# Kernel tuning notes

Hardware: AMD Instinct MI355X
Metric: run time of the kernel (lower is better)

Reference implementation:

```python
import jax, jax.numpy as jnp
import numpy as np

F32 = jnp.float32

def denorm_px(pts, H, W):
    # kornia denormalize_pixel_coordinates: [-1,1] -> pixel
    x = (pts[..., 0] + 1.0) * (W - 1) * 0.5
    y = (pts[..., 1] + 1.0) * (H - 1) * 0.5
    return jnp.stack([x, y], axis=-1)

def norm_px(pts, H, W):
    x = pts[..., 0] * 2.0 / (W - 1) - 1.0
    y = pts[..., 1] * 2.0 / (H - 1) - 1.0
    return jnp.stack([x, y], axis=-1)

def conv2d_same(x, k, mode):
    # depthwise 2d conv, 'same' output, border via jnp.pad mode
    kh, kw = k.shape
    ph, pw = kh // 2, kw // 2
    xp = jnp.pad(x, ((0, 0), (0, 0), (ph, ph), (pw, pw)), mode=mode)
    C = x.shape[1]
    kern = jnp.broadcast_to(k[None, None], (C, 1, kh, kw)).astype(x.dtype)
    return jax.lax.conv_general_dilated(xp, kern, (1, 1), 'VALID',
        dimension_numbers=('NCHW', 'OIHW', 'NCHW'), feature_group_count=C)

def nms2d(x, k=5):
    p = k // 2
    m = jax.lax.reduce_window(x, -jnp.inf, jax.lax.max, (1, 1, k, k), (1, 1, 1, 1),
                              [(0, 0), (0, 0), (p, p), (p, p)])
    return jnp.where(x == m, x, 0.0)

def gaussian_kernel2d(ksize=7, sigma=1.0):
    ax = jnp.arange(ksize, dtype=F32) - (ksize - 1) / 2.0
    g = jnp.exp(-0.5 * (ax / sigma) ** 2)
    g = g / g.sum()
    return jnp.outer(g, g)

def gftt_response(gray):
    # kornia CornerGFTT: normalized sobel grads, blurred structure tensor, min-eig
    sx = jnp.array([[-1, 0, 1], [-2, 0, 2], [-1, 0, 1]], F32) / 8.0
    gx = conv2d_same(gray, sx, 'edge')
    gy = conv2d_same(gray, sx.T, 'edge')
    g = gaussian_kernel2d(7, 1.0)
    dx2 = conv2d_same(gx * gx, g, 'reflect')
    dy2 = conv2d_same(gy * gy, g, 'reflect')
    dxy = conv2d_same(gx * gy, g, 'reflect')
    tr = dx2 + dy2
    disc = jnp.sqrt(jnp.clip((dx2 - dy2) ** 2 + 4.0 * dxy ** 2, 0.0))
    return 0.5 * (tr - disc)

def laplacian5(x):
    k = jnp.ones((5, 5), F32).at[2, 2].set(1.0 - 25.0)
    k = k / jnp.abs(k).sum()  # kornia normalized laplacian kernel
    return conv2d_same(x, k, 'reflect')

def pairwise_project(pts, depths, poses, K):
    # pts [B,N,2] normalized; poses [B,4,4] cam-to-world
    # returns proj [B(dst),B(src),N,2] normalized + vis [B,B,N]
    B, N, _ = pts.shape
    H, W = depths.shape[-2:]
    px = denorm_px(pts, H, W)
    xi = jnp.clip(jnp.round(px[..., 0]), 0, W - 1).astype(jnp.int32)
    yi = jnp.clip(jnp.round(px[..., 1]), 0, H - 1).astype(jnp.int32)
    d = depths[jnp.arange(B)[:, None], 0, yi, xi]  # [B,N]
    Kinv = jnp.linalg.inv(K)
    hom = jnp.concatenate([px, jnp.ones_like(px[..., :1])], axis=-1)
    cam = (hom @ Kinv.T) * d[..., None]  # [B,N,3]
    R, t = poses[:, :3, :3], poses[:, :3, 3]
    world = jnp.einsum('bij,bnj->bni', R, cam) + t[:, None]
    diff = world[None] - t[:, None, None]  # [i,j,n,3]
    cam2 = jnp.einsum('iab,ijna->ijnb', R, diff)  # R_i^T (world - t_i)
    uvw = cam2 @ K.T
    z = uvw[..., 2]
    zs = jnp.where(jnp.abs(z) > 1e-6, z, 1e-6)
    u, v = uvw[..., 0] / zs, uvw[..., 1] / zs
    vis = (z > 0.1) & (u >= 0) & (u <= W - 1) & (v >= 0) & (v <= H - 1)
    return norm_px(jnp.stack([u, v], -1), H, W), vis

def pairwise_cosine_inter(x, y, eps=1e-8):
    xx = jnp.sum(x * x, -1)
    yy = jnp.sum(y * y, -1)
    xy = jnp.einsum('amd,bnd->abmn', x, y)
    den = jnp.sqrt(jnp.clip(xx[:, None, :, None] * yy[None, :, None, :], eps * eps))
    return xy / den

def pairwise_cosine_intra(x, y, eps=1e-8):
    xx = jnp.sum(x * x, -1)
    yy = jnp.sum(y * y, -1)
    xy = jnp.einsum('bmd,bnd->bmn', x, y)
    den = jnp.sqrt(jnp.clip(xx[..., :, None] * yy[..., None, :], eps * eps))
    return xy / den

def distinction_loss(desc):
    return jnp.maximum(pairwise_cosine_intra(desc, desc), 0.0).mean()

def match_loss(desc, points, proj, vis, H, W, radius=1.0):
    B, N, _ = points.shape
    src = denorm_px(jax.lax.stop_gradient(points), H, W)  # [b,m,2]
    dst = denorm_px(jax.lax.stop_gradient(proj), H, W)  # [a,b,n,2]
    x2 = jnp.sum(src * src, -1)  # [b,m]
    y2 = jnp.sum(dst * dst, -1)  # [a,b,n]
    xy = jnp.einsum('bmd,abnd->abmn', src, dst)
    dist = jnp.sqrt(jnp.clip(x2[None, :, :, None] + y2[:, :, None, :] - 2.0 * xy, 0.0))
    valid = vis[:, :, :, None]  # torch: dist[invis rows] = nan -> excluded from both masks
    tri = jnp.triu(jnp.ones((N, N), bool), 1)
    pcos = pairwise_cosine_inter(desc, desc)
    mpos = (dist <= radius) & tri & valid
    mneg = (dist > radius) & tri & valid
    pos_mean = jnp.sum(jnp.where(mpos, pcos, 0.0)) / jnp.maximum(mpos.sum(), 1)
    neg_mean = jnp.sum(jnp.where(mneg, pcos, 0.0)) / jnp.maximum(mneg.sum(), 1)
    return 1.0 - pos_mean + neg_mean

def get_corner_target(imgs, depths, poses, K, num_corners=500, radius=8):
    B, _, H, W = imgs.shape
    gray = 0.299 * imgs[:, 0:1] + 0.587 * imgs[:, 1:2] + 0.114 * imgs[:, 2:3]
    corners = nms2d(gftt_response(gray), 5)
    # MaxPool(8, return_indices) + MaxUnpool(8): keep only per-8x8-block max
    xr = corners.reshape(B, 1, H // radius, radius, W // radius, radius)
    bm = xr.max(axis=(3, 5), keepdims=True)
    keep = jnp.where(xr == bm, xr, 0.0).reshape(B, 1, H, W)
    values, idx = jax.lax.top_k(keep.reshape(B, -1), num_corners)  # [B,Nc]
    coords = jnp.stack([idx % W, idx // W], axis=2).astype(F32)  # (x,y)
    coords = norm_px(coords, H, W)
    proj, vis = pairwise_project(coords, depths, poses, K)  # [B,B,Nc,2]
    proj = jnp.where(vis[..., None], proj, -2.0)
    comb = jnp.transpose(proj, (1, 0, 2, 3)).reshape(B, B * num_corners, 2)
    px = jnp.round(denorm_px(comb, H, W)).astype(jnp.int32)
    wf = px[..., 0].reshape(-1)
    hf = px[..., 1].reshape(-1)
    bf = jnp.repeat(jnp.arange(B), B * num_corners)
    vals = jnp.tile(values.reshape(-1), B)
    mask = (wf >= 0) & (hf >= 0) & (wf < W) & (hf < H)
    vals = jnp.where(mask, vals, 0.0)
    wf = jnp.clip(wf, 0, W - 1)
    hf = jnp.clip(hf, 0, H - 1)
    target = jnp.zeros_like(corners).at[bf, 0, hf, wf].max(vals)
    target = nms2d(target, 5)
    return jax.lax.stop_gradient((target > 0).astype(F32))

def score_loss(scores, imgs, depths, poses, K):
    target = get_corner_target(imgs, depths, poses, K)
    p = jnp.clip(scores, 1e-12, 1.0 - 1e-12)
    bce = -(target * jnp.log(p) + (1.0 - target) * jnp.log(1.0 - p)).mean()
    lap = laplacian5(scores)
    return bce + (scores * jnp.exp(-lap)).mean() * 10.0

def featurenet_loss(descriptors, points, pointness, depths_dense, poses, K, imgs):
    beta = (1.0, 0.5, 1.0)
    H, W = pointness.shape[2], pointness.shape[3]
    distinction = distinction_loss(descriptors)
    cornerness = score_loss(pointness, imgs, depths_dense, poses, K)
    proj_pts, vis = pairwise_project(points, depths_dense, poses, K)
    match = match_loss(descriptors, points, proj_pts, vis, H, W, radius=1.0)
    return beta[0] * distinction + beta[1] * cornerness + beta[2] * match

def setup_inputs() -> dict:
    key = jax.random.key(0)
    ks = jax.random.split(key, 6)
    B, N, D, H, W = 6, 1024, 128, 320, 320
    descriptors = jax.random.normal(ks[0], (B, N, D), F32)
    points = jax.random.uniform(ks[1], (B, N, 2), F32, -0.9, 0.9)
    pointness = jax.random.uniform(ks[2], (B, 1, H, W), F32, 1e-3, 1.0 - 1e-3)
    depths_dense = jax.random.uniform(ks[3], (B, 1, H, W), F32, 1.0, 6.0)
    t = jax.random.uniform(ks[4], (B, 3), F32, -0.2, 0.2)
    poses = jnp.tile(jnp.eye(4, dtype=F32), (B, 1, 1)).at[:, :3, 3].set(t)
    K = jnp.array([[float(W), 0.0, W / 2.0], [0.0, float(W), H / 2.0], [0.0, 0.0, 1.0]], F32)
    imgs = jax.random.uniform(ks[5], (B, 3, H, W), F32)
    return dict(descriptors=descriptors, points=points, pointness=pointness,
                depths_dense=depths_dense, poses=poses, K=K, imgs=imgs)

def reference(descriptors, points, pointness, depths_dense, poses, K, imgs):
    return featurenet_loss(descriptors, points, pointness, depths_dense, poses, K, imgs)
```

## Files before the change

### kernel.cpp

```cpp
#include <hip/hip_runtime.h>
#include <stdint.h>

#define BB 6
#define NPTS 1024
#define DD 128
#define HH 320
#define WW 320
#define NC 500
#define HWsz (HH*WW)
#define CAP 2048
#define NBLK ((HH/8)*(WW/8))
#define TX 32
#define TY 8
#define NSLOT 64

typedef __attribute__((ext_vector_type(8))) short bf16x8;
typedef __attribute__((ext_vector_type(4))) float f32x4;

__device__ __forceinline__ int clampi(int v, int lo, int hi){ return v<lo?lo:(v>hi?hi:v); }
__device__ __forceinline__ int refl(int p, int L){ if(p<0)p=-p; if(p>=L)p=2*L-2-p; return p; }

__device__ __forceinline__ float wave_sum(float v){
  #pragma unroll
  for (int o = 32; o > 0; o >>= 1) v += __shfl_xor(v, o, 64);
  return v;
}
__device__ __forceinline__ double wave_sumd(double v){
  #pragma unroll
  for (int o = 32; o > 0; o >>= 1) v += __shfl_xor(v, o, 64);
  return v;
}
__device__ __forceinline__ float wave_max(float v){
  #pragma unroll
  for (int o = 32; o > 0; o >>= 1) v = fmaxf(v, __shfl_xor(v, o, 64));
  return v;
}

__device__ __constant__ float GW[7] = {
  0.0044330481f, 0.0540055850f, 0.2420362300f, 0.3990502700f,
  0.2420362300f, 0.0540055850f, 0.0044330481f };

struct Proj { float u, v; int vis; };

__device__ Proj project_point(float ptx, float pty, int jsrc, int itgt,
                              const float* __restrict__ depths,
                              const float* __restrict__ poses,
                              const float* __restrict__ Km)
{
  float pxx = ((ptx + 1.0f)*(float)(WW-1))*0.5f;
  float pxy = ((pty + 1.0f)*(float)(HH-1))*0.5f;
  float rx = rintf(pxx), ry = rintf(pxy);
  rx = fminf(fmaxf(rx, 0.f), (float)(WW-1));
  ry = fminf(fmaxf(ry, 0.f), (float)(HH-1));
  int xi = (int)rx, yi = (int)ry;
  float d = depths[(size_t)jsrc*HWsz + yi*WW + xi];
  float a00=Km[0],a01=Km[1],a02=Km[2],a10=Km[3],a11=Km[4],a12=Km[5],a20=Km[6],a21=Km[7],a22=Km[8];
  float det = a00*(a11*a22 - a12*a21) - a01*(a10*a22 - a12*a20) + a02*(a10*a21 - a11*a20);
  float id_ = 1.0f/det;
  float i00 = (a11*a22 - a12*a21)*id_;
  float i01 = (a02*a21 - a01*a22)*id_;
  float i02 = (a01*a12 - a02*a11)*id_;
  float i10 = (a12*a20 - a10*a22)*id_;
  float i11 = (a00*a22 - a02*a20)*id_;
  float i12 = (a02*a10 - a00*a12)*id_;
  float i20 = (a10*a21 - a11*a20)*id_;
  float i21 = (a01*a20 - a00*a21)*id_;
  float i22 = (a00*a11 - a01*a10)*id_;
  float c0 = (i00*pxx + i01*pxy + i02)*d;
  float c1 = (i10*pxx + i11*pxy + i12)*d;
  float c2 = (i20*pxx + i21*pxy + i22)*d;
  const float* Pj = poses + (size_t)jsrc*16;
  float w0 = Pj[0]*c0 + Pj[1]*c1 + Pj[2]*c2  + Pj[3];
  float w1 = Pj[4]*c0 + Pj[5]*c1 + Pj[6]*c2  + Pj[7];
  float w2 = Pj[8]*c0 + Pj[9]*c1 + Pj[10]*c2 + Pj[11];
  const float* Pi = poses + (size_t)itgt*16;
  float dx = w0 - Pi[3], dy = w1 - Pi[7], dz = w2 - Pi[11];
  float e0 = Pi[0]*dx + Pi[4]*dy + Pi[8]*dz;
  float e1 = Pi[1]*dx + Pi[5]*dy + Pi[9]*dz;
  float e2 = Pi[2]*dx + Pi[6]*dy + Pi[10]*dz;
  float uu = a00*e0 + a01*e1 + a02*e2;
  float vv = a10*e0 + a11*e1 + a12*e2;
  float zz = a20*e0 + a21*e1 + a22*e2;
  float zs = (fabsf(zz) > 1e-6f) ? zz : 1e-6f;
  Proj r;
  r.u = uu/zs; r.v = vv/zs;
  r.vis = (zz > 0.1f) && (r.u >= 0.f) && (r.u <= (float)(WW-1)) && (r.v >= 0.f) && (r.v <= (float)(HH-1));
  return r;
}

__global__ __launch_bounds__(256) void k_gftt(const float* __restrict__ imgs,
        float* __restrict__ resp){
  __shared__ float lg[TY+8][TX+8];
  __shared__ float lxx[TY+6][TX+6], lyy[TY+6][TX+6], lxy[TY+6][TX+6];
  int b = blockIdx.z;
  int x0 = blockIdx.x*TX, y0 = blockIdx.y*TY;
  const float* br = imgs + (size_t)b*3*HWsz;
  const float* bg = br + HWsz;
  const float* bbl = bg + HWsz;
  const int GW2 = TX+8, GH2 = TY+8;
  for (int i = threadIdx.x; i < GH2*GW2; i += 256){
    int ly = i / GW2, lx = i - ly*GW2;
    int gy = clampi(y0-4+ly, 0, HH-1), gx = clampi(x0-4+lx, 0, WW-1);
    size_t off = (size_t)gy*WW + gx;
    lg[ly][lx] = 0.299f*br[off] + 0.587f*bg[off] + 0.114f*bbl[off];
  }
  __syncthreads();
  const int PW2 = TX+6, PH2 = TY+6;
  for (int i = threadIdx.x; i < PH2*PW2; i += 256){
    int ly = i / PW2, lx = i - ly*PW2;
    int pcy = refl(y0-3+ly, HH), pcx = refl(x0-3+lx, WW);
    int ym = clampi(pcy-1,0,HH-1)-(y0-4), yc = pcy-(y0-4), yp = clampi(pcy+1,0,HH-1)-(y0-4);
    int xm = clampi(pcx-1,0,WW-1)-(x0-4), xc = pcx-(x0-4), xp = clampi(pcx+1,0,WW-1)-(x0-4);
    float g00=lg[ym][xm], g01=lg[ym][xc], g02=lg[ym][xp];
    float g10=lg[yc][xm],                 g12=lg[yc][xp];
    float g20=lg[yp][xm], g21=lg[yp][xc], g22=lg[yp][xp];
    float gx = 0.125f*(g02-g00)+0.25f*(g12-g10)+0.125f*(g22-g20);
    float gy = 0.125f*(g20-g00)+0.25f*(g21-g01)+0.125f*(g22-g02);
    lxx[ly][lx]=gx*gx; lyy[ly][lx]=gy*gy; lxy[ly][lx]=gx*gy;
  }
  __syncthreads();
  int tx = threadIdx.x & (TX-1), ty = threadIdx.x / TX;
  float sxx=0.f, syy=0.f, sxy=0.f;
  #pragma unroll
  for (int i=0;i<7;++i){
    float wr = GW[i];
    #pragma unroll
    for (int j=0;j<7;++j){
      float wc = wr*GW[j];
      sxx += wc*lxx[ty+i][tx+j];
      syy += wc*lyy[ty+i][tx+j];
      sxy += wc*lxy[ty+i][tx+j];
    }
  }
  float tr = sxx+syy, df = sxx-syy;
  float disc = sqrtf(fmaxf(df*df + 4.f*sxy*sxy, 0.f));
  resp[(size_t)b*HWsz + (size_t)(y0+ty)*WW + (x0+tx)] = 0.5f*(tr - disc);
}

__global__ __launch_bounds__(256) void k_nmsblk(const float* __restrict__ resp,
        unsigned long long* __restrict__ ckeys, unsigned int* __restrict__ ccnt){
  __shared__ float lr[TY+4][TX+4];
  __shared__ float lk[TY][TX];
  int b = blockIdx.z;
  int x0 = blockIdx.x*TX, y0 = blockIdx.y*TY;
  const float* rb = resp + (size_t)b*HWsz;
  const int W2 = TX+4, H2 = TY+4;
  for (int i = threadIdx.x; i < H2*W2; i += 256){
    int ly = i / W2, lx = i - ly*W2;
    int gy = y0 - 2 + ly, gx = x0 - 2 + lx;
    lr[ly][lx] = (gy >= 0 && gy < HH && gx >= 0 && gx < WW) ? rb[(size_t)gy*WW + gx] : -1e30f;
  }
  __syncthreads();
  int tx = threadIdx.x & (TX-1), ty = threadIdx.x / TX;
  float m = -1e30f;
  #pragma unroll
  for (int dy=0; dy<5; ++dy)
    #pragma unroll
    for (int dx=0; dx<5; ++dx) m = fmaxf(m, lr[ty+dy][tx+dx]);
  float r = lr[ty+2][tx+2];
  lk[ty][tx] = (r == m) ? r : 0.f;
  __syncthreads();
  int wave = threadIdx.x >> 6, lane = threadIdx.x & 63;
  int ly = lane >> 3, lx = wave*8 + (lane & 7);
  float v = lk[ly][lx];
  float bm = wave_max(v);
  if (!(bm > 0.f)) return;
  unsigned long long mask = __ballot(v == bm);
  if (v == bm){
    int yy = y0 + ly, xx2 = x0 + lx;
    unsigned long long key =
      ((unsigned long long)__float_as_uint(bm) << 32) |
      (unsigned long long)(0xFFFFFFFFu - (unsigned int)(yy*WW + xx2));
    int rank = __popcll(mask & ((1ull << lane) - 1ull));
    int rblk = blockIdx.y*(WW/8) + blockIdx.x*4 + wave;
    if (rank == 0){
      ckeys[(size_t)b*CAP + rblk] = key;
    } else {
      unsigned int slot = NBLK + atomicAdd(&ccnt[b], 1u);
      if (slot < CAP) ckeys[(size_t)b*CAP + slot] = key;
    }
  }
}

__global__ __launch_bounds__(1024) void k_top500(const unsigned long long* __restrict__ ckeys,
        float* __restrict__ cpts, float* __restrict__ cvals){
  __shared__ unsigned long long sk[CAP];
  int b = blockIdx.x;
  int tid = threadIdx.x;
  for (int i = tid; i < CAP; i += 1024)
    sk[i] = ckeys[(size_t)b*CAP + i];
  __syncthreads();
  for (int k = 2; k <= CAP; k <<= 1){
    for (int j = k >> 1; j > 0; j >>= 1){
      for (int i = tid; i < CAP; i += 1024){
        int l = i ^ j;
        if (l > i){
          unsigned long long A = sk[i], Bv = sk[l];
          bool up = ((i & k) == 0);
          if ((A > Bv) == up){ sk[i] = Bv; sk[l] = A; }
        }
      }
      __syncthreads();
    }
  }
  if (tid < NC){
    unsigned long long key = sk[CAP-1-tid];
    float val = __uint_as_float((unsigned int)(key >> 32));
    size_t o = (size_t)b*NC + tid;
    if (val > 0.f){
      unsigned int idx = 0xFFFFFFFFu - (unsigned int)(key & 0xFFFFFFFFull);
      float fx = (float)(idx % WW), fy = (float)(idx / WW);
      cpts[o*2+0] = (fx*2.0f)/(float)(WW-1) - 1.0f;
      cpts[o*2+1] = (fy*2.0f)/(float)(HH-1) - 1.0f;
      cvals[o] = val;
    } else {
      cpts[o*2+0] = __int_as_float(0x7fc00000);
      cpts[o*2+1] = __int_as_float(0x7fc00000);
      cvals[o] = 0.f;
    }
  }
}

__global__ void k_corner_scatter(const float* __restrict__ cpts, const float* __restrict__ cvals,
        const float* __restrict__ depths, const float* __restrict__ poses,
        const float* __restrict__ Km, unsigned int* __restrict__ target){
  int t = blockIdx.x*blockDim.x + threadIdx.x;
  if (t >= BB*BB*NC) return;
  int i = t / (BB*NC); int r = t - i*(BB*NC); int j = r / NC; int n = r - j*NC;
  float val = cvals[(size_t)i*NC + n];
  float ptx = cpts[((size_t)j*NC+n)*2+0];
  float pty = cpts[((size_t)j*NC+n)*2+1];
  if (!(val > 0.f) || ptx != ptx) return;
  Proj pr = project_point(ptx, pty, j, i, depths, poses, Km);
  if (!pr.vis) return;
  float nu = (pr.u*2.0f)/(float)(WW-1) - 1.0f;
  float nv = (pr.v*2.0f)/(float)(HH-1) - 1.0f;
  float px2 = ((nu+1.0f)*(float)(WW-1))*0.5f;
  float py2 = ((nv+1.0f)*(float)(HH-1))*0.5f;
  float rx = rintf(px2), ry = rintf(py2);
  if (!(rx >= 0.f && ry >= 0.f && rx <= (float)(WW-1) && ry <= (float)(HH-1))) return;
  int wf = (int)rx, hf = (int)ry;
  atomicMax(&target[(size_t)j*HWsz + hf*WW + wf], __float_as_uint(val));
}

__global__ __launch_bounds__(256) void k_score_reduce(const float* __restrict__ target,
        const float* __restrict__ scores, double* __restrict__ accs){
  __shared__ float ltg[TY+4][TX+4], lsc[TY+4][TX+4];
  __shared__ float rbuf[4][2];
  int b = blockIdx.z;
  int x0 = blockIdx.x*TX, y0 = blockIdx.y*TY;
  const float* tg = target + (size_t)b*HWsz;
  const float* sb = scores + (size_t)b*HWsz;
  const int W2 = TX+4, H2 = TY+4;
  for (int i = threadIdx.x; i < H2*W2; i += 256){
    int ly = i / W2, lx = i - ly*W2;
    int gy = y0 - 2 + ly, gx = x0 - 2 + lx;
    ltg[ly][lx] = (gy >= 0 && gy < HH && gx >= 0 && gx < WW) ? tg[(size_t)gy*WW + gx] : -1e30f;
    lsc[ly][lx] = sb[(size_t)refl(gy,HH)*WW + refl(gx,WW)];
  }
  __syncthreads();
  int tx = threadIdx.x & (TX-1), ty = threadIdx.x / TX;
  float m = -1e30f, S5 = 0.f;
  #pragma unroll
  for (int dy=0; dy<5; ++dy)
    #pragma unroll
    for (int dx=0; dx<5; ++dx){
      m = fmaxf(m, ltg[ty+dy][tx+dx]);
      S5 += lsc[ty+dy][tx+dx];
    }
  float tv = ltg[ty+2][tx+2];
  float sc = lsc[ty+2][tx+2];
  float tb = (tv > 0.f && tv == m) ? 1.f : 0.f;
  float pc = fminf(fmaxf(sc, 1e-12f), 1.0f - 1e-12f);
  float bce = -(tb*logf(pc) + (1.f-tb)*logf(1.f-pc));
  float lap = (S5 - sc)*(1.0f/48.0f) - 0.5f*sc;
  float extra = sc*expf(-lap);
  bce = wave_sum(bce); extra = wave_sum(extra);
  int wave = threadIdx.x >> 6, lane = threadIdx.x & 63;
  if (lane == 0){ rbuf[wave][0] = bce; rbuf[wave][1] = extra; }
  __syncthreads();
  if (threadIdx.x == 0){
    int slot = (blockIdx.x + blockIdx.y*(WW/TX) + blockIdx.z*400) & (NSLOT-1);
    atomicAdd(&accs[(1*NSLOT + slot)*8], (double)(rbuf[0][0]+rbuf[1][0]+rbuf[2][0]+rbuf[3][0]));
    atomicAdd(&accs[(2*NSLOT + slot)*8], (double)(rbuf[0][1]+rbuf[1][1]+rbuf[2][1]+rbuf[3][1]));
  }
}

__global__ void k_rowproj(const float* __restrict__ desc, float* __restrict__ xx,
        unsigned short* __restrict__ dbf,
        const float* __restrict__ points, const float* __restrict__ depths,
        const float* __restrict__ poses, const float* __restrict__ Km,
        float* __restrict__ mproj, unsigned char* __restrict__ mvis){
  int t = blockIdx.x*blockDim.x + threadIdx.x;
  if (t < BB*NPTS){
    const float* dptr = desc + (size_t)t*DD;
    unsigned short* optr = dbf + (size_t)t*DD;
    float s = 0.f;
    for (int d = 0; d < DD; d += 4){
      float4 v = *(const float4*)(dptr + d);
      s += v.x*v.x + v.y*v.y + v.z*v.z + v.w*v.w;
      unsigned int u0 = __float_as_uint(v.x); optr[d+0] = (unsigned short)((u0 + 0x7fffu + ((u0>>16)&1u)) >> 16);
      unsigned int u1 = __float_as_uint(v.y); optr[d+1] = (unsigned short)((u1 + 0x7fffu + ((u1>>16)&1u)) >> 16);
      unsigned int u2 = __float_as_uint(v.z); optr[d+2] = (unsigned short)((u2 + 0x7fffu + ((u2>>16)&1u)) >> 16);
      unsigned int u3 = __float_as_uint(v.w); optr[d+3] = (unsigned short)((u3 + 0x7fffu + ((u3>>16)&1u)) >> 16);
    }
    xx[t] = s;
    return;
  }
  int t2 = t - BB*NPTS;
  if (t2 >= BB*BB*NPTS) return;
  int i = t2 / (BB*NPTS); int r = t2 - i*(BB*NPTS); int j = r / NPTS; int n = r - j*NPTS;
  float ptx = points[((size_t)j*NPTS+n)*2+0];
  float pty = points[((size_t)j*NPTS+n)*2+1];
  Proj pr = project_point(ptx, pty, j, i, depths, poses, Km);
  mproj[(size_t)t2*2+0] = (pr.u*2.0f)/(float)(WW-1) - 1.0f;
  mproj[(size_t)t2*2+1] = (pr.v*2.0f)/(float)(HH-1) - 1.0f;
  mvis[t2] = pr.vis ? 1 : 0;
}

__global__ __launch_bounds__(256) void k_grams(const unsigned short* __restrict__ dbf,
        const float* __restrict__ xx, const float* __restrict__ points,
        const float* __restrict__ mproj, const unsigned char* __restrict__ mvis,
        double* __restrict__ accs){
  __shared__ float rbuf[4][4];
  int ab = blockIdx.z; int a = ab / BB, b = ab - a*BB;
  int ti = blockIdx.x;
  int mt = 0;
  while (ti >= 8 - mt){ ti -= 8 - mt; ++mt; }
  int nt = mt + ti;
  int tid = threadIdx.x;
  int wave = tid >> 6, lane = tid & 63;
  int wr = mt*128 + (wave&1)*64;
  int wc = nt*128 + (wave>>1)*64;
  int r = lane & 15, kg = lane >> 4;
  const unsigned short* descA = dbf + (size_t)a*NPTS*DD;
  const unsigned short* descB = dbf + (size_t)b*NPTS*DD;
  const float* xxa = xx + (size_t)a*NPTS;
  const float* xxb = xx + (size_t)b*NPTS;
  const float* pts = points + (size_t)b*NPTS*2;
  const float* mp  = mproj + (((size_t)a*BB+b)*NPTS)*2;
  const unsigned char* mv = mvis + ((size_t)a*BB+b)*NPTS;
  f32x4 acc[4][4] = {};
  #pragma unroll
  for (int ks = 0; ks < 4; ++ks){
    int ko = ks*32 + kg*8;
    bf16x8 af[4], bf[4];
    #pragma unroll
    for (int q = 0; q < 4; ++q){
      af[q] = *(const bf16x8*)(descA + (size_t)(wr+q*16+r)*DD + ko);
      bf[q] = *(const bf16x8*)(descB + (size_t)(wc+q*16+r)*DD + ko);
    }
    #pragma unroll
    for (int mi = 0; mi < 4; ++mi)
      #pragma unroll
      for (int ni = 0; ni < 4; ++ni)
        acc[mi][ni] = __builtin_amdgcn_mfma_f32_16x16x32_bf16(af[mi], bf[ni], acc[mi][ni], 0, 0, 0);
  }
  float nxxv[4], ndx[4], ndy[4], ny2[4];
  #pragma unroll
  for (int ni = 0; ni < 4; ++ni){
    int n = wc + ni*16 + r;
    nxxv[ni] = xxb[n];
    float qx = mp[n*2+0], qy = mp[n*2+1];
    float dx = ((qx+1.f)*(float)(WW-1))*0.5f;
    float dy = ((qy+1.f)*(float)(HH-1))*0.5f;
    ndx[ni] = dx; ndy[ni] = dy;
    ny2[ni] = dx*dx + dy*dy;
  }
  float pos = 0.f, neg = 0.f, pcf = 0.f, ncf = 0.f;
  #pragma unroll
  for (int mi = 0; mi < 4; ++mi){
    #pragma unroll
    for (int j = 0; j < 4; ++j){
      int m = wr + mi*16 + 4*kg + j;
      if (!mv[m]) continue;
      float px = pts[m*2+0], py = pts[m*2+1];
      float sx = ((px+1.f)*(float)(WW-1))*0.5f;
      float sy = ((py+1.f)*(float)(HH-1))*0.5f;
      float x2 = sx*sx + sy*sy;
      float xm = xxa[m];
      #pragma unroll
      for (int ni = 0; ni < 4; ++ni){
        int n = wc + ni*16 + r;
        if (m >= n) continue;
        float dv = acc[mi][ni][j];
        float d2 = x2 + ny2[ni] - 2.f*(sx*ndx[ni] + sy*ndy[ni]);
        float p = dv * rsqrtf(fmaxf(xm * nxxv[ni], 1e-16f));
        if (d2 <= 1.0f){ pos += p; pcf += 1.f; }
        else           { neg += p; ncf += 1.f; }
      }
    }
  }
  pos = wave_sum(pos); neg = wave_sum(neg);
  pcf = wave_sum(pcf); ncf = wave_sum(ncf);
  if (lane == 0){ rbuf[wave][0] = pos; rbuf[wave][1] = neg; rbuf[wave][2] = pcf; rbuf[wave][3] = ncf; }
  __syncthreads();
  if (tid == 0){
    int slot = (blockIdx.x + blockIdx.z*8) & (NSLOT-1);
    atomicAdd(&accs[(3*NSLOT + slot)*8], (double)(rbuf[0][0]+rbuf[1][0]+rbuf[2][0]+rbuf[3][0]));
    atomicAdd(&accs[(4*NSLOT + slot)*8], (double)(rbuf[0][1]+rbuf[1][1]+rbuf[2][1]+rbuf[3][1]));
    atomicAdd(&accs[(5*NSLOT + slot)*8], (double)(rbuf[0][2]+rbuf[1][2]+rbuf[2][2]+rbuf[3][2]));
    atomicAdd(&accs[(6*NSLOT + slot)*8], (double)(rbuf[0][3]+rbuf[1][3]+rbuf[2][3]+rbuf[3][3]));
  }
  int flat = blockIdx.x + 36*blockIdx.z;
  if (flat >= 384) return;
  int db = flat >> 6;
  int dt = flat & 63;
  int wr2 = (dt >> 3)*128 + (wave&1)*64;
  int wc2 = (dt & 7)*128 + (wave>>1)*64;
  const unsigned short* descb = dbf + (size_t)db*NPTS*DD;
  const float* xb = xx + (size_t)db*NPTS;
  f32x4 ec[4][4] = {};
  #pragma unroll
  for (int ks = 0; ks < 4; ++ks){
    int ko = ks*32 + kg*8;
    bf16x8 af[4], bf[4];
    #pragma unroll
    for (int q = 0; q < 4; ++q){
      af[q] = *(const bf16x8*)(descb + (size_t)(wr2+q*16+r)*DD + ko);
      bf[q] = *(const bf16x8*)(descb + (size_t)(wc2+q*16+r)*DD + ko);
    }
    #pragma unroll
    for (int mi = 0; mi < 4; ++mi)
      #pragma unroll
      for (int ni = 0; ni < 4; ++ni)
        ec[mi][ni] = __builtin_amdgcn_mfma_f32_16x16x32_bf16(af[mi], bf[ni], ec[mi][ni], 0, 0, 0);
  }
  float xn[4];
  #pragma unroll
  for (int ni = 0; ni < 4; ++ni) xn[ni] = xb[wc2 + ni*16 + r];
  float local = 0.f;
  #pragma unroll
  for (int mi = 0; mi < 4; ++mi){
    #pragma unroll
    for (int j = 0; j < 4; ++j){
      float xm = xb[wr2 + mi*16 + 4*kg + j];
      #pragma unroll
      for (int ni = 0; ni < 4; ++ni)
        local += fmaxf(ec[mi][ni][j] * rsqrtf(fmaxf(xm*xn[ni], 1e-16f)), 0.f);
    }
  }
  local = wave_sum(local);
  __syncthreads();
  if (lane == 0) rbuf[wave][0] = local;
  __syncthreads();
  if (tid == 0){
    int slot = flat & (NSLOT-1);
    atomicAdd(&accs[(0*NSLOT + slot)*8], (double)(rbuf[0][0]+rbuf[1][0]+rbuf[2][0]+rbuf[3][0]));
  }
}

__global__ void k_final(const double* __restrict__ accs, float* __restrict__ out){
  int lane = threadIdx.x;
  double tot[7];
  #pragma unroll
  for (int q = 0; q < 7; ++q)
    tot[q] = wave_sumd(accs[((size_t)q*NSLOT + lane)*8]);
  if (lane == 0){
    double distinction = tot[0] / (double)((long long)BB*NPTS*NPTS);
    double bce = tot[1] / (double)((long long)BB*HWsz);
    double extra = tot[2] / (double)((long long)BB*HWsz);
    double cornerness = bce + 10.0*extra;
    double pcd = tot[5] < 0.5 ? 1.0 : tot[5];
    double ncd = tot[6] < 0.5 ? 1.0 : tot[6];
    double pos_mean = tot[3] / pcd;
    double neg_mean = tot[4] / ncd;
    double match = 1.0 - pos_mean + neg_mean;
    out[0] = (float)(distinction + 0.5*cornerness + match);
  }
}

extern "C" void kernel_launch(void* const* d_in, const int* in_sizes, int n_in,
                              void* d_out, int out_size, void* d_ws, size_t ws_size,
                              hipStream_t stream) {
  (void)in_sizes; (void)n_in; (void)out_size; (void)ws_size;
  const float* desc   = (const float*)d_in[0];
  const float* points = (const float*)d_in[1];
  const float* scores = (const float*)d_in[2];
  const float* depths = (const float*)d_in[3];
  const float* poses  = (const float*)d_in[4];
  const float* Km     = (const float*)d_in[5];
  const float* imgs   = (const float*)d_in[6];
  float* out = (float*)d_out;

  const size_t S = (size_t)BB*HWsz;
  float* resp   = (float*)d_ws;
  float* target = resp + S;
  unsigned long long* ckeys = (unsigned long long*)(target + S);
  unsigned int* ccnt = (unsigned int*)(ckeys + (size_t)BB*CAP);
  double* accs = (double*)(ccnt + 8);
  float* cpts  = (float*)(accs + 7*NSLOT*8);
  float* cvals = cpts + (size_t)BB*NC*2;
  float* xx    = cvals + (size_t)BB*NC;
  float* mproj = xx + (size_t)BB*NPTS;
  unsigned char* mvis = (unsigned char*)(mproj + (size_t)BB*BB*NPTS*2);
  unsigned short* dbf = (unsigned short*)(mvis + (size_t)BB*BB*NPTS);

  dim3 blk(256);
  dim3 gtile(WW/TX, HH/TY, BB);

  hipMemsetAsync(target, 0,
      S*sizeof(float) +
      (size_t)BB*CAP*sizeof(unsigned long long) + 8*sizeof(unsigned int) +
      (size_t)7*NSLOT*8*sizeof(double), stream);

  k_gftt<<<gtile, blk, 0, stream>>>(imgs, resp);
  k_nmsblk<<<gtile, blk, 0, stream>>>(resp, ckeys, ccnt);
  k_top500<<<dim3(BB), dim3(1024), 0, stream>>>(ckeys, cpts, cvals);
  {
    int n = BB*BB*NC;
    k_corner_scatter<<<dim3((n+255)/256), blk, 0, stream>>>(cpts, cvals, depths, poses, Km,
                                                            (unsigned int*)target);
  }
  k_score_reduce<<<gtile, blk, 0, stream>>>(target, scores, accs);
  {
    int n = BB*NPTS + BB*BB*NPTS;
    k_rowproj<<<dim3((n+255)/256), blk, 0, stream>>>(desc, xx, dbf, points, depths, poses, Km,
                                                     mproj, mvis);
  }
  k_grams<<<dim3(36, 1, BB*BB), blk, 0, stream>>>(dbf, xx, points, mproj, mvis, accs);
  k_final<<<dim3(1), dim3(64), 0, stream>>>(accs, out);
}
```

Measured before the change: 193.0 us.

## Fold rowproj into gftt launch and finalize via last-block ticket in grams

The descriptor bf16 conversion and projection work now runs as extra blocks of the gftt kernel, and its standalone launch is removed. The final reduction moves into k_grams: each block takes a ticket and the last one sums the accumulators and writes the output, so k_final is no longer launched. The score kernel also switches to fast __logf/__expf intrinsics. The aim is to cut launch overhead and serial tiny-kernel gaps, at the cost of a threadfence/atomic ticket protocol and slightly less accurate transcendentals.

Measured after the change: 199.9 us. +3.6%, slower.

```diff
diff --git a/kernel.cpp b/kernel.cpp
--- a/kernel.cpp
+++ b/kernel.cpp
@@ -89,11 +89,45 @@
 }
 
 __global__ __launch_bounds__(256) void k_gftt(const float* __restrict__ imgs,
-        float* __restrict__ resp){
+        float* __restrict__ resp,
+        const float* __restrict__ desc, float* __restrict__ xx, unsigned short* __restrict__ dbf,
+        const float* __restrict__ points, const float* __restrict__ depths,
+        const float* __restrict__ poses, const float* __restrict__ Km,
+        float* __restrict__ mproj, unsigned char* __restrict__ mvis){
   __shared__ float lg[TY+8][TX+8];
   __shared__ float lxx[TY+6][TX+6], lyy[TY+6][TX+6], lxy[TY+6][TX+6];
-  int b = blockIdx.z;
-  int x0 = blockIdx.x*TX, y0 = blockIdx.y*TY;
+  int fb = blockIdx.x;
+  if (fb >= 2400){
+    int t = (fb - 2400)*256 + threadIdx.x;
+    if (t < BB*NPTS){
+      const float* dptr = desc + (size_t)t*DD;
+      unsigned short* optr = dbf + (size_t)t*DD;
+      float s = 0.f;
+      for (int d = 0; d < DD; d += 4){
+        float4 v = *(const float4*)(dptr + d);
+        s += v.x*v.x + v.y*v.y + v.z*v.z + v.w*v.w;
+        unsigned int u0 = __float_as_uint(v.x); optr[d+0] = (unsigned short)((u0 + 0x7fffu + ((u0>>16)&1u)) >> 16);
+        unsigned int u1 = __float_as_uint(v.y); optr[d+1] = (unsigned short)((u1 + 0x7fffu + ((u1>>16)&1u)) >> 16);
+        unsigned int u2 = __float_as_uint(v.z); optr[d+2] = (unsigned short)((u2 + 0x7fffu + ((u2>>16)&1u)) >> 16);
+        unsigned int u3 = __float_as_uint(v.w); optr[d+3] = (unsigned short)((u3 + 0x7fffu + ((u3>>16)&1u)) >> 16);
+      }
+      xx[t] = s;
+      return;
+    }
+    int t2 = t - BB*NPTS;
+    if (t2 >= BB*BB*NPTS) return;
+    int i = t2 / (BB*NPTS); int r = t2 - i*(BB*NPTS); int j = r / NPTS; int n = r - j*NPTS;
+    float ptx = points[((size_t)j*NPTS+n)*2+0];
+    float pty = points[((size_t)j*NPTS+n)*2+1];
+    Proj pr = project_point(ptx, pty, j, i, depths, poses, Km);
+    mproj[(size_t)t2*2+0] = (pr.u*2.0f)/(float)(WW-1) - 1.0f;
+    mproj[(size_t)t2*2+1] = (pr.v*2.0f)/(float)(HH-1) - 1.0f;
+    mvis[t2] = pr.vis ? 1 : 0;
+    return;
+  }
+  int b = fb / 400; int rem = fb - b*400;
+  int by = rem / 10, bx = rem - by*10;
+  int x0 = bx*TX, y0 = by*TY;
   const float* br = imgs + (size_t)b*3*HWsz;
   const float* bg = br + HWsz;
   const float* bbl = bg + HWsz;
@@ -272,9 +306,9 @@
   float sc = lsc[ty+2][tx+2];
   float tb = (tv > 0.f && tv == m) ? 1.f : 0.f;
   float pc = fminf(fmaxf(sc, 1e-12f), 1.0f - 1e-12f);
-  float bce = -(tb*logf(pc) + (1.f-tb)*logf(1.f-pc));
+  float bce = -(tb*__logf(pc) + (1.f-tb)*__logf(1.f-pc));
   float lap = (S5 - sc)*(1.0f/48.0f) - 0.5f*sc;
-  float extra = sc*expf(-lap);
+  float extra = sc*__expf(-lap);
   bce = wave_sum(bce); extra = wave_sum(extra);
   int wave = threadIdx.x >> 6, lane = threadIdx.x & 63;
   if (lane == 0){ rbuf[wave][0] = bce; rbuf[wave][1] = extra; }
@@ -286,43 +320,13 @@
   }
 }
 
-__global__ void k_rowproj(const float* __restrict__ desc, float* __restrict__ xx,
-        unsigned short* __restrict__ dbf,
-        const float* __restrict__ points, const float* __restrict__ depths,
-        const float* __restrict__ poses, const float* __restrict__ Km,
-        float* __restrict__ mproj, unsigned char* __restrict__ mvis){
-  int t = blockIdx.x*blockDim.x + threadIdx.x;
-  if (t < BB*NPTS){
-    const float* dptr = desc + (size_t)t*DD;
-    unsigned short* optr = dbf + (size_t)t*DD;
-    float s = 0.f;
-    for (int d = 0; d < DD; d += 4){
-      float4 v = *(const float4*)(dptr + d);
-      s += v.x*v.x + v.y*v.y + v.z*v.z + v.w*v.w;
-      unsigned int u0 = __float_as_uint(v.x); optr[d+0] = (unsigned short)((u0 + 0x7fffu + ((u0>>16)&1u)) >> 16);
-      unsigned int u1 = __float_as_uint(v.y); optr[d+1] = (unsigned short)((u1 + 0x7fffu + ((u1>>16)&1u)) >> 16);
-      unsigned int u2 = __float_as_uint(v.z); optr[d+2] = (unsigned short)((u2 + 0x7fffu + ((u2>>16)&1u)) >> 16);
-      unsigned int u3 = __float_as_uint(v.w); optr[d+3] = (unsigned short)((u3 + 0x7fffu + ((u3>>16)&1u)) >> 16);
-    }
-    xx[t] = s;
-    return;
-  }
-  int t2 = t - BB*NPTS;
-  if (t2 >= BB*BB*NPTS) return;
-  int i = t2 / (BB*NPTS); int r = t2 - i*(BB*NPTS); int j = r / NPTS; int n = r - j*NPTS;
-  float ptx = points[((size_t)j*NPTS+n)*2+0];
-  float pty = points[((size_t)j*NPTS+n)*2+1];
-  Proj pr = project_point(ptx, pty, j, i, depths, poses, Km);
-  mproj[(size_t)t2*2+0] = (pr.u*2.0f)/(float)(WW-1) - 1.0f;
-  mproj[(size_t)t2*2+1] = (pr.v*2.0f)/(float)(HH-1) - 1.0f;
-  mvis[t2] = pr.vis ? 1 : 0;
-}
-
 __global__ __launch_bounds__(256) void k_grams(const unsigned short* __restrict__ dbf,
         const float* __restrict__ xx, const float* __restrict__ points,
         const float* __restrict__ mproj, const unsigned char* __restrict__ mvis,
-        double* __restrict__ accs){
+        double* __restrict__ accs, unsigned int* __restrict__ ticket,
+        float* __restrict__ out){
   __shared__ float rbuf[4][4];
+  __shared__ int lastFlag;
   int ab = blockIdx.z; int a = ab / BB, b = ab - a*BB;
   int ti = blockIdx.x;
   int mt = 0;
@@ -403,70 +407,76 @@
     atomicAdd(&accs[(6*NSLOT + slot)*8], (double)(rbuf[0][3]+rbuf[1][3]+rbuf[2][3]+rbuf[3][3]));
   }
   int flat = blockIdx.x + 36*blockIdx.z;
-  if (flat >= 384) return;
-  int db = flat >> 6;
-  int dt = flat & 63;
-  int wr2 = (dt >> 3)*128 + (wave&1)*64;
-  int wc2 = (dt & 7)*128 + (wave>>1)*64;
-  const unsigned short* descb = dbf + (size_t)db*NPTS*DD;
-  const float* xb = xx + (size_t)db*NPTS;
-  f32x4 ec[4][4] = {};
-  #pragma unroll
-  for (int ks = 0; ks < 4; ++ks){
-    int ko = ks*32 + kg*8;
-    bf16x8 af[4], bf[4];
-    #pragma unroll
-    for (int q = 0; q < 4; ++q){
-      af[q] = *(const bf16x8*)(descb + (size_t)(wr2+q*16+r)*DD + ko);
-      bf[q] = *(const bf16x8*)(descb + (size_t)(wc2+q*16+r)*DD + ko);
-    }
-    #pragma unroll
-    for (int mi = 0; mi < 4; ++mi)
+  if (flat < 384){
+    int db = flat >> 6;
+    int dt = flat & 63;
+    int wr2 = (dt >> 3)*128 + (wave&1)*64;
+    int wc2 = (dt & 7)*128 + (wave>>1)*64;
+    const unsigned short* descb = dbf + (size_t)db*NPTS*DD;
+    const float* xb = xx + (size_t)db*NPTS;
+    f32x4 ec[4][4] = {};
+    #pragma unroll
+    for (int ks = 0; ks < 4; ++ks){
+      int ko = ks*32 + kg*8;
+      bf16x8 af[4], bf[4];
       #pragma unroll
-      for (int ni = 0; ni < 4; ++ni)
-        ec[mi][ni] = __builtin_amdgcn_mfma_f32_16x16x32_bf16(af[mi], bf[ni], ec[mi][ni], 0, 0, 0);
-  }
-  float xn[4];
-  #pragma unroll
-  for (int ni = 0; ni < 4; ++ni) xn[ni] = xb[wc2 + ni*16 + r];
-  float local = 0.f;
-  #pragma unroll
-  for (int mi = 0; mi < 4; ++mi){
-    #pragma unroll
-    for (int j = 0; j < 4; ++j){
-      float xm = xb[wr2 + mi*16 + 4*kg + j];
+      for (int q = 0; q < 4; ++q){
+        af[q] = *(const bf16x8*)(descb + (size_t)(wr2+q*16+r)*DD + ko);
+        bf[q] = *(const bf16x8*)(descb + (size_t)(wc2+q*16+r)*DD + ko);
+      }
       #pragma unroll
-      for (int ni = 0; ni < 4; ++ni)
-        local += fmaxf(ec[mi][ni][j] * rsqrtf(fmaxf(xm*xn[ni], 1e-16f)), 0.f);
-    }
-  }
-  local = wave_sum(local);
-  __syncthreads();
-  if (lane == 0) rbuf[wave][0] = local;
-  __syncthreads();
+      for (int mi = 0; mi < 4; ++mi)
+        #pragma unroll
+        for (int ni = 0; ni < 4; ++ni)
+          ec[mi][ni] = __builtin_amdgcn_mfma_f32_16x16x32_bf16(af[mi], bf[ni], ec[mi][ni], 0, 0, 0);
+    }
+    float xn[4];
+    #pragma unroll
+    for (int ni = 0; ni < 4; ++ni) xn[ni] = xb[wc2 + ni*16 + r];
+    float local = 0.f;
+    #pragma unroll
+    for (int mi = 0; mi < 4; ++mi){
+      #pragma unroll
+      for (int j = 0; j < 4; ++j){
+        float xm = xb[wr2 + mi*16 + 4*kg + j];
+        #pragma unroll
+        for (int ni = 0; ni < 4; ++ni)
+          local += fmaxf(ec[mi][ni][j] * rsqrtf(fmaxf(xm*xn[ni], 1e-16f)), 0.f);
+      }
+    }
+    local = wave_sum(local);
+    __syncthreads();
+    if (lane == 0) rbuf[wave][0] = local;
+    __syncthreads();
+    if (tid == 0){
+      int slot = flat & (NSLOT-1);
+      atomicAdd(&accs[(0*NSLOT + slot)*8], (double)(rbuf[0][0]+rbuf[1][0]+rbuf[2][0]+rbuf[3][0]));
+    }
+  }
   if (tid == 0){
-    int slot = flat & (NSLOT-1);
-    atomicAdd(&accs[(0*NSLOT + slot)*8], (double)(rbuf[0][0]+rbuf[1][0]+rbuf[2][0]+rbuf[3][0]));
-  }
-}
-
-__global__ void k_final(const double* __restrict__ accs, float* __restrict__ out){
-  int lane = threadIdx.x;
-  double tot[7];
-  #pragma unroll
-  for (int q = 0; q < 7; ++q)
-    tot[q] = wave_sumd(accs[((size_t)q*NSLOT + lane)*8]);
-  if (lane == 0){
-    double distinction = tot[0] / (double)((long long)BB*NPTS*NPTS);
-    double bce = tot[1] / (double)((long long)BB*HWsz);
-    double extra = tot[2] / (double)((long long)BB*HWsz);
-    double cornerness = bce + 10.0*extra;
-    double pcd = tot[5] < 0.5 ? 1.0 : tot[5];
-    double ncd = tot[6] < 0.5 ? 1.0 : tot[6];
-    double pos_mean = tot[3] / pcd;
-    double neg_mean = tot[4] / ncd;
-    double match = 1.0 - pos_mean + neg_mean;
-    out[0] = (float)(distinction + 0.5*cornerness + match);
+    __threadfence();
+    unsigned int old = atomicAdd(ticket, 1u);
+    lastFlag = (old == 36u*36u - 1u) ? 1 : 0;
+  }
+  __syncthreads();
+  if (lastFlag && wave == 0){
+    double tot[7];
+    #pragma unroll
+    for (int q = 0; q < 7; ++q)
+      tot[q] = wave_sumd(__hip_atomic_load(&accs[((size_t)q*NSLOT + lane)*8],
+                                           __ATOMIC_RELAXED, __HIP_MEMORY_SCOPE_AGENT));
+    if (lane == 0){
+      double distinction = tot[0] / (double)((long long)BB*NPTS*NPTS);
+      double bce = tot[1] / (double)((long long)BB*HWsz);
+      double extra = tot[2] / (double)((long long)BB*HWsz);
+      double cornerness = bce + 10.0*extra;
+      double pcd = tot[5] < 0.5 ? 1.0 : tot[5];
+      double ncd = tot[6] < 0.5 ? 1.0 : tot[6];
+      double pos_mean = tot[3] / pcd;
+      double neg_mean = tot[4] / ncd;
+      double match = 1.0 - pos_mean + neg_mean;
+      out[0] = (float)(distinction + 0.5*cornerness + match);
+    }
   }
 }
 
@@ -504,7 +514,8 @@
       (size_t)BB*CAP*sizeof(unsigned long long) + 8*sizeof(unsigned int) +
       (size_t)7*NSLOT*8*sizeof(double), stream);
 
-  k_gftt<<<gtile, blk, 0, stream>>>(imgs, resp);
+  k_gftt<<<dim3(2400 + 168), blk, 0, stream>>>(imgs, resp, desc, xx, dbf,
+                                               points, depths, poses, Km, mproj, mvis);
   k_nmsblk<<<gtile, blk, 0, stream>>>(resp, ckeys, ccnt);
   k_top500<<<dim3(BB), dim3(1024), 0, stream>>>(ckeys, cpts, cvals);
   {
@@ -513,11 +524,6 @@
                                                             (unsigned int*)target);
   }
   k_score_reduce<<<gtile, blk, 0, stream>>>(target, scores, accs);
-  {
-    int n = BB*NPTS + BB*BB*NPTS;
-    k_rowproj<<<dim3((n+255)/256), blk, 0, stream>>>(desc, xx, dbf, points, depths, poses, Km,
-                                                     mproj, mvis);
-  }
-  k_grams<<<dim3(36, 1, BB*BB), blk, 0, stream>>>(dbf, xx, points, mproj, mvis, accs);
-  k_final<<<dim3(1), dim3(64), 0, stream>>>(accs, out);
-}
+  k_grams<<<dim3(36, 1, BB*BB), blk, 0, stream>>>(dbf, xx, points, mproj, mvis, accs,
+                                                  &ccnt[6], out);
+}
```
